# Performance work log

Hardware: AMD Instinct MI355X
Metric: run time of the kernel (lower is better)

Reference implementation:

```python
import jax, jax.numpy as jnp
import numpy as np

B, S, D, H = 4, 2048, 1024, 16
d = D // H
SCALE = d ** -0.5


def setup_inputs() -> dict:
    key = jax.random.key(0)
    k1, k2, k3 = jax.random.split(key, 3)
    x = jax.random.normal(k1, (B, S, D), dtype=jnp.float32)
    # causal keep-mask (True = keep), shape (B, 1, S, S)
    causal = jnp.tril(jnp.ones((S, S), dtype=bool))
    mask = jnp.broadcast_to(causal[None, None, :, :], (B, 1, S, S))
    # nn.Linear(D, 3D, bias=False): weight (3D, D); out_proj weight (D, D)
    w_qkv = jax.random.normal(k2, (3 * D, D), dtype=jnp.float32) * (D ** -0.5)
    w_out = jax.random.normal(k3, (D, D), dtype=jnp.float32) * (D ** -0.5)
    return {"x": x, "mask": mask, "w_qkv": w_qkv, "w_out": w_out}


def reference(x, mask, w_qkv, w_out):
    # qkv projection: y = x @ W^T, split into q, k, v
    qkv = jnp.einsum('bsd,ed->bse', x, w_qkv)  # (B, S, 3D)
    q, k, v = jnp.split(qkv, 3, axis=-1)
    # (B, S, H, d) -> (B, H, S, d)
    q = q.reshape(B, S, H, d).transpose(0, 2, 1, 3)
    k = k.reshape(B, S, H, d).transpose(0, 2, 1, 3)
    v = v.reshape(B, S, H, d).transpose(0, 2, 1, 3)
    # scores (B, H, S, S)
    attn = jnp.einsum('bhqd,bhkd->bhqk', q, k) * SCALE
    attn = jnp.where(mask, attn, -jnp.inf)
    attn = jax.nn.softmax(attn, axis=-1)
    out = jnp.einsum('bhqk,bhkd->bhqd', attn, v)
    out = out.transpose(0, 2, 1, 3).reshape(B, S, D)
    out = jnp.einsum('bsd,ed->bse', out, w_out)
    return out, (k, v)
```

## Files before the change

kernel.cpp:

```cpp
#include <hip/hip_runtime.h>
#include <hip/hip_bf16.h>

typedef __bf16 bf16_t;
typedef bf16_t bf16x8 __attribute__((ext_vector_type(8)));
typedef bf16_t bf16x4 __attribute__((ext_vector_type(4)));
typedef float  f32x4  __attribute__((ext_vector_type(4)));
typedef float  f32x8  __attribute__((ext_vector_type(8)));
typedef float  f32x16 __attribute__((ext_vector_type(16)));

#define B_  4
#define S_  2048
#define D_  1024
#define H_  16
#define HD  64

#define QSCALE 0.1803368801111204f

#define KV_TILE_ELEMS 4096
#define KV_BH_ELEMS   262144

__device__ __forceinline__ void async_copy16(const void* g, void* l) {
    __builtin_amdgcn_global_load_lds((const __attribute__((address_space(1))) void*)g,
                                     (__attribute__((address_space(3))) void*)l,
                                     16, 0, 0);
}

__device__ __forceinline__ float fast_exp2(float x) {
    float r;
    asm("v_exp_f32 %0, %1" : "=v"(r) : "v"(x));
    return r;
}

__global__ __launch_bounds__(256) void cvt_kernel(const float* __restrict__ in,
                                                  bf16_t* __restrict__ out, int n4) {
    int i = blockIdx.x * 256 + threadIdx.x;
    if (i >= n4) return;
    float4 f = ((const float4*)in)[i];
    bf16x4 o = { (bf16_t)f.x, (bf16_t)f.y, (bf16_t)f.z, (bf16_t)f.w };
    ((bf16x4*)out)[i] = o;
}

__device__ __forceinline__ void gemm_tile(const bf16_t* __restrict__ A,
                                          const bf16_t* __restrict__ Bt,
                                          int lda, int ldb, int m0, int n0, int K,
                                          bf16_t* As, bf16_t* Bs, f32x4 acc[4][4]) {
    const int lane = threadIdx.x & 63;
    const int wv   = threadIdx.x >> 6;
    const int wm   = wv >> 1, wn = wv & 1;
    const int r8   = lane >> 3, c8 = lane & 7;
    const int lo   = lane & 15, hi = lane >> 4;
    const int swz  = (lo & 7) * 8;
    const int csw  = (c8 ^ (r8 & 7)) * 8;

    for (int k0 = 0; k0 < K; k0 += 64) {
        #pragma unroll
        for (int i = 0; i < 4; ++i) {
            const int c   = wv * 4 + i;
            const int row = c * 8 + r8;
            async_copy16(A  + (size_t)(m0 + row) * lda + k0 + csw, As + c * 512);
            async_copy16(Bt + (size_t)(n0 + row) * ldb + k0 + csw, Bs + c * 512);
        }
        __syncthreads();
        #pragma unroll
        for (int kk = 0; kk < 2; ++kk) {
            const int kos = (kk * 32 + hi * 8) ^ swz;
            bf16x8 aF[4], bF[4];
            #pragma unroll
            for (int m = 0; m < 4; ++m)
                aF[m] = *(const bf16x8*)(As + (wm * 64 + m * 16 + lo) * 64 + kos);
            #pragma unroll
            for (int n = 0; n < 4; ++n)
                bF[n] = *(const bf16x8*)(Bs + (wn * 64 + n * 16 + lo) * 64 + kos);
            #pragma unroll
            for (int m = 0; m < 4; ++m)
                #pragma unroll
                for (int n = 0; n < 4; ++n)
                    acc[m][n] = __builtin_amdgcn_mfma_f32_16x16x32_bf16(aF[m], bF[n], acc[m][n], 0, 0, 0);
        }
        __syncthreads();
    }
}

__global__ __launch_bounds__(256) void gemm_qkv_kernel(const bf16_t* __restrict__ A,
                                                       const bf16_t* __restrict__ Bt,
                                                       float* __restrict__ out,
                                                       bf16_t* __restrict__ q_ws,
                                                       bf16_t* __restrict__ kv_frag) {
    __shared__ __align__(16) bf16_t As[128 * 64];
    __shared__ __align__(16) bf16_t Bs[128 * 64];
    const int m0 = blockIdx.y * 128, n0 = blockIdx.x * 128;
    const f32x4 zero = {0.f, 0.f, 0.f, 0.f};
    f32x4 acc[4][4];
    #pragma unroll
    for (int m = 0; m < 4; ++m)
        #pragma unroll
        for (int n = 0; n < 4; ++n) acc[m][n] = zero;

    gemm_tile(A, Bt, D_, D_, m0, n0, D_, As, Bs, acc);

    const int lane = threadIdx.x & 63, wv = threadIdx.x >> 6;
    const int wm = wv >> 1, wn = wv & 1;
    const int lo = lane & 15, hi = lane >> 4;
    #pragma unroll
    for (int m = 0; m < 4; ++m) {
        #pragma unroll
        for (int n = 0; n < 4; ++n) {
            const int gcol = n0 + wn * 64 + n * 16 + lo;
            const int sec  = gcol >> 10;
            const int e    = gcol & 1023;
            const int h    = e >> 6, dv = e & 63;
            #pragma unroll
            for (int j4 = 0; j4 < 4; ++j4) {
                const int grow = m0 + wm * 64 + m * 16 + hi * 4 + j4;
                const float v  = acc[m][n][j4];
                const int b = grow >> 11, s = grow & 2047;
                const size_t idx2 = ((((size_t)b * H_ + h) * S_ + s) << 6) + dv;
                if (sec == 0) {
                    q_ws[idx2] = (bf16_t)(v * QSCALE);
                } else if (sec == 1) {
                    out[8388608u + idx2] = v;
                    const int bh   = b * H_ + h;
                    const int tile = s >> 5, ql = s & 31;
                    const int c    = dv >> 4, hb = (dv >> 3) & 1, jj = dv & 7;
                    kv_frag[(((size_t)bh * 64 + tile) * 8 + c) * 512 + hb * 256 + ql * 8 + jj] = (bf16_t)v;
                } else {
                    out[16777216u + idx2] = v;
                }
            }
        }
    }
}

__global__ __launch_bounds__(256) void build_vfrag_kernel(const float* __restrict__ v_f32,
                                                          bf16_t* __restrict__ kv_frag) {
    __shared__ __align__(16) bf16_t T[64][72];
    const int bh = blockIdx.x;
    const int s0 = blockIdx.y * 64;
    const int t  = threadIdx.x;
    {
        const int sl  = t >> 2;
        const int dv0 = (t & 3) * 16;
        const float* src = v_f32 + ((size_t)bh * S_ + s0 + sl) * HD + dv0;
        float tmp[16];
        #pragma unroll
        for (int i = 0; i < 4; ++i) *(float4*)(tmp + i * 4) = ((const float4*)src)[i];
        #pragma unroll
        for (int i = 0; i < 16; ++i) T[dv0 + i][sl] = (bf16_t)tmp[i];
    }
    __syncthreads();
    {
        const int st = t >> 7;
        const int r  = t & 127;
        const int cc = r >> 5;
        const int l  = r & 31;
        const int khi = cc >> 1, hd = cc & 1;
        const int d   = hd * 32 + l;
        const int tile = (s0 >> 5) + st;
        bf16_t* dst = kv_frag + (((size_t)bh * 64 + tile) * 8 + 4 + cc) * 512 + l * 8;
        const int slb = st * 32 + khi * 16;
        *(bf16x8*)(dst)       = *(const bf16x8*)&T[d][slb];
        *(bf16x8*)(dst + 256) = *(const bf16x8*)&T[d][slb + 8];
    }
}

__global__ __launch_bounds__(256) void attn_kernel(const bf16_t* __restrict__ q_ws,
                                                   const bf16_t* __restrict__ kv_frag,
                                                   bf16_t* __restrict__ attn_ws) {
    __shared__ __align__(16) float MRG[2][2][64][20];
    __shared__ float LSUM[2][64];
    __shared__ __align__(16) bf16_t T[2][32][72];
    const int lane = threadIdx.x & 63;
    const int wv   = threadIdx.x >> 6;
    const int blk   = blockIdx.x;
    const int x     = blk & 7;
    const int r     = blk >> 3;
    const int bh    = x + 8 * (r & 7);
    const int pr    = wv >> 1;
    const int khalf = wv & 1;
    const int p     = (r >> 3) * 2 + pr;

    const int ql = lane & 31;
    const int hb = lane >> 5;
    const size_t kv_base = (size_t)bh * (S_ * HD);
    const int b = bh >> 4, h = bh & 15;

    const bf16_t* kvb = kv_frag + (size_t)bh * KV_BH_ELEMS + (size_t)lane * 8;

    auto load_k = [&](int tile, bf16x8 kf[4]) {
        const bf16_t* tp = kvb + (size_t)tile * KV_TILE_ELEMS;
        #pragma unroll
        for (int c = 0; c < 4; ++c) kf[c] = *(const bf16x8*)(tp + c * 512);
    };
    auto load_v = [&](int tile, bf16x8 vf[4]) {
        const bf16_t* tp = kvb + (size_t)tile * KV_TILE_ELEMS + 2048;
        #pragma unroll
        for (int i = 0; i < 4; ++i) vf[i] = *(const bf16x8*)(tp + i * 512);
    };

    #pragma unroll 1
    for (int pass = 0; pass < 2; ++pass) {
        const int qblock = pass ? (63 - p) : p;
        const int q0 = qblock * 32;
        const int nt  = qblock + 1;
        const int mid = nt >> 1;
        const int tstart = khalf ? mid : 0;
        const int tend   = khalf ? nt  : mid;

        bf16x8 qF[4];
        const bf16_t* qrow = q_ws + kv_base + (size_t)(q0 + ql) * HD + hb * 8;
        #pragma unroll
        for (int c = 0; c < 4; ++c) qF[c] = *(const bf16x8*)(qrow + 16 * c);

        f32x16 accT0 = {}, accT1 = {};
        float lsum = 0.f;

        auto compute_tile = [&](const bf16x8 kf[4], const bf16x8 vf[4], bool diag) {
            f32x16 s = {};
            #pragma unroll
            for (int c = 0; c < 4; ++c)
                s = __builtin_amdgcn_mfma_f32_32x32x16_bf16(kf[c], qF[c], s, 0, 0, 0);
            if (diag) {
                #pragma unroll
                for (int rr = 0; rr < 16; ++rr) {
                    const int kloc = (rr & 3) + 8 * (rr >> 2) + 4 * hb;
                    if (kloc > ql) s[rr] = -1e30f;
                }
            }
            #pragma unroll
            for (int rr = 0; rr < 16; ++rr) s[rr] = fast_exp2(s[rr]);
            f32x8 t8 = __builtin_shufflevector(s, s, 0, 1, 2, 3, 4, 5, 6, 7) +
                       __builtin_shufflevector(s, s, 8, 9, 10, 11, 12, 13, 14, 15);
            f32x4 t4 = __builtin_shufflevector(t8, t8, 0, 1, 2, 3) +
                       __builtin_shufflevector(t8, t8, 4, 5, 6, 7);
            lsum += (t4[0] + t4[1]) + (t4[2] + t4[3]);

            unsigned w[8];
            #pragma unroll
            for (int i = 0; i < 8; ++i) {
                unsigned d;
                asm("v_cvt_pk_bf16_f32 %0, %1, %2" : "=v"(d) : "v"(s[2 * i]), "v"(s[2 * i + 1]));
                w[i] = d;
            }
            union { unsigned u[4]; bf16x8 v; } pf0, pf1;
            {
                auto r0 = __builtin_amdgcn_permlane32_swap(w[0], w[2], false, false);
                auto r1 = __builtin_amdgcn_permlane32_swap(w[1], w[3], false, false);
                pf0.u[0] = r0[0]; pf0.u[1] = r1[0]; pf0.u[2] = r0[1]; pf0.u[3] = r1[1];
            }
            {
                auto r0 = __builtin_amdgcn_permlane32_swap(w[4], w[6], false, false);
                auto r1 = __builtin_amdgcn_permlane32_swap(w[5], w[7], false, false);
                pf1.u[0] = r0[0]; pf1.u[1] = r1[0]; pf1.u[2] = r0[1]; pf1.u[3] = r1[1];
            }

            accT0 = __builtin_amdgcn_mfma_f32_32x32x16_bf16(vf[0], pf0.v, accT0, 0, 0, 0);
            accT1 = __builtin_amdgcn_mfma_f32_32x32x16_bf16(vf[1], pf0.v, accT1, 0, 0, 0);
            accT0 = __builtin_amdgcn_mfma_f32_32x32x16_bf16(vf[2], pf1.v, accT0, 0, 0, 0);
            accT1 = __builtin_amdgcn_mfma_f32_32x32x16_bf16(vf[3], pf1.v, accT1, 0, 0, 0);
        };

        int t = tstart;
        for (; t + 1 < tend; t += 2) {
            bf16x8 kA[4], vA[4], kB[4], vB[4];
            load_k(t, kA);
            load_v(t, vA);
            load_k(t + 1, kB);
            load_v(t + 1, vB);
            compute_tile(kA, vA, t == qblock);
            compute_tile(kB, vB, (t + 1) == qblock);
        }
        if (t < tend) {
            bf16x8 kA[4], vA[4];
            load_k(t, kA);
            load_v(t, vA);
            compute_tile(kA, vA, t == qblock);
        }

        if (khalf) {
            *(f32x16*)&MRG[pr][0][lane][0] = accT0;
            *(f32x16*)&MRG[pr][1][lane][0] = accT1;
            LSUM[pr][lane] = lsum;
        }
        __syncthreads();
        if (!khalf) {
            accT0 += *(const f32x16*)&MRG[pr][0][lane][0];
            accT1 += *(const f32x16*)&MRG[pr][1][lane][0];
            lsum  += LSUM[pr][lane];
            const float ltot = lsum + __shfl_xor(lsum, 32, 64);
            const float inv  = 1.0f / ltot;
            #pragma unroll
            for (int rr = 0; rr < 16; ++rr) {
                const int dl = (rr & 3) + 8 * (rr >> 2) + 4 * hb;
                T[pr][ql][dl]      = (bf16_t)(accT0[rr] * inv);
                T[pr][ql][32 + dl] = (bf16_t)(accT1[rr] * inv);
            }
            asm volatile("s_waitcnt lgkmcnt(0)" ::: "memory");
            #pragma unroll
            for (int it = 0; it < 4; ++it) {
                const int ch  = it * 64 + lane;
                const int row = ch >> 3, c8 = ch & 7;
                bf16x8 o = *(const bf16x8*)&T[pr][row][c8 * 8];
                *(bf16x8*)(attn_ws + ((size_t)(b * S_ + q0 + row)) * D_ + h * HD + c8 * 8) = o;
            }
        }
        __syncthreads();
    }
}

__global__ __launch_bounds__(256) void gemm_out_kernel(const bf16_t* __restrict__ A,
                                                       const bf16_t* __restrict__ Bt,
                                                       float* __restrict__ out) {
    __shared__ __align__(16) bf16_t As[128 * 64];
    __shared__ __align__(16) bf16_t Bs[128 * 64];
    const int bid = blockIdx.x;
    const int xcd = bid & 7, idx = bid >> 3;
    const int m0 = idx * 128, n0 = xcd * 128;
    const f32x4 zero = {0.f, 0.f, 0.f, 0.f};
    f32x4 acc[4][4];
    #pragma unroll
    for (int m = 0; m < 4; ++m)
        #pragma unroll
        for (int n = 0; n < 4; ++n) acc[m][n] = zero;

    gemm_tile(A, Bt, D_, D_, m0, n0, D_, As, Bs, acc);

    const int lane = threadIdx.x & 63, wv = threadIdx.x >> 6;
    const int wm = wv >> 1, wn = wv & 1;
    const int lo = lane & 15, hi = lane >> 4;
    #pragma unroll
    for (int m = 0; m < 4; ++m) {
        #pragma unroll
        for (int n = 0; n < 4; ++n) {
            const int gcol = n0 + wn * 64 + n * 16 + lo;
            #pragma unroll
            for (int j = 0; j < 4; ++j) {
                const int grow = m0 + wm * 64 + m * 16 + hi * 4 + j;
                out[(size_t)grow * D_ + gcol] = acc[m][n][j];
            }
        }
    }
}

extern "C" void kernel_launch(void* const* d_in, const int* in_sizes, int n_in,
                              void* d_out, int out_size, void* d_ws, size_t ws_size,
                              hipStream_t stream) {
    (void)in_sizes; (void)n_in; (void)out_size; (void)ws_size;
    const float* x     = (const float*)d_in[0];
    const float* w_qkv = (const float*)d_in[2];
    const float* w_out = (const float*)d_in[3];
    float* out = (float*)d_out;
    char* ws = (char*)d_ws;

    bf16_t* x_bf    = (bf16_t*)(ws);
    bf16_t* wqkv_bf = (bf16_t*)(ws + 16777216);
    bf16_t* wout_bf = (bf16_t*)(ws + 23068672);
    bf16_t* q_ws    = (bf16_t*)(ws + 25165824);
    bf16_t* kv_frag = (bf16_t*)(ws + 41943040);
    bf16_t* attn_ws = (bf16_t*)(ws + 75497472);

    cvt_kernel<<<8192, 256, 0, stream>>>(x, x_bf, 2097152);
    cvt_kernel<<<3072, 256, 0, stream>>>(w_qkv, wqkv_bf, 786432);
    cvt_kernel<<<1024, 256, 0, stream>>>(w_out, wout_bf, 262144);

    gemm_qkv_kernel<<<dim3(24, 64), 256, 0, stream>>>(x_bf, wqkv_bf, out, q_ws, kv_frag);
    build_vfrag_kernel<<<dim3(64, 32), 256, 0, stream>>>(out + 16777216, kv_frag);
    attn_kernel<<<1024, 256, 0, stream>>>(q_ws, kv_frag, attn_ws);
    gemm_out_kernel<<<512, 256, 0, stream>>>(attn_ws, wout_bf, out);
}
```

Before: 183.8 us.

## Triple-buffer GEMM k-loop with async LDS loads and enlarge tiles to 256x128

Restructures the shared GEMM core into a three-stage software pipeline: async global-to-LDS copies for tiles t+1..t+3 are issued while tile t is computed, with explicit vmcnt waits and raw barriers in place of a load-then-sync loop. Block tile grows to 256x128 with 512 threads (8 waves), which halves the grid for both projection GEMMs and drops the XCD-aware block mapping in the output GEMM. This aims to hide global load latency, but uses 144 KB of LDS per block, which limits occupancy to one block per CU, and the hand-written vmcnt counts must exactly match the number of copies issued.

```diff
diff --git a/kernel.cpp b/kernel.cpp
--- a/kernel.cpp
+++ b/kernel.cpp
@@ -18,6 +18,10 @@
 
 #define KV_TILE_ELEMS 4096
 #define KV_BH_ELEMS   262144
+
+#define BM 256
+#define BN 128
+#define BK 64
 
 __device__ __forceinline__ void async_copy16(const void* g, void* l) {
     __builtin_amdgcn_global_load_lds((const __attribute__((address_space(1))) void*)g,
@@ -40,7 +44,7 @@
     ((bf16x4*)out)[i] = o;
 }
 
-__device__ __forceinline__ void gemm_tile(const bf16_t* __restrict__ A,
+__device__ __forceinline__ void gemm_core(const bf16_t* __restrict__ A,
                                           const bf16_t* __restrict__ Bt,
                                           int lda, int ldb, int m0, int n0, int K,
                                           bf16_t* As, bf16_t* Bs, f32x4 acc[4][4]) {
@@ -50,53 +54,78 @@
     const int r8   = lane >> 3, c8 = lane & 7;
     const int lo   = lane & 15, hi = lane >> 4;
     const int swz  = (lo & 7) * 8;
-    const int csw  = (c8 ^ (r8 & 7)) * 8;
-
-    for (int k0 = 0; k0 < K; k0 += 64) {
+    const int csw  = (c8 ^ r8) * 8;
+
+    auto stage = [&](int t, int db) {
+        const int k0 = t * BK;
+        bf16_t* as = As + db * (BM * BK);
+        bf16_t* bs = Bs + db * (BN * BK);
         #pragma unroll
         for (int i = 0; i < 4; ++i) {
-            const int c   = wv * 4 + i;
-            const int row = c * 8 + r8;
-            async_copy16(A  + (size_t)(m0 + row) * lda + k0 + csw, As + c * 512);
-            async_copy16(Bt + (size_t)(n0 + row) * ldb + k0 + csw, Bs + c * 512);
-        }
-        __syncthreads();
+            const int row = i * 64 + wv * 8 + r8;
+            async_copy16(A + (size_t)(m0 + row) * lda + k0 + csw, as + (i * 64 + wv * 8) * BK);
+        }
+        #pragma unroll
+        for (int i = 0; i < 2; ++i) {
+            const int row = i * 64 + wv * 8 + r8;
+            async_copy16(Bt + (size_t)(n0 + row) * ldb + k0 + csw, bs + (i * 64 + wv * 8) * BK);
+        }
+    };
+
+    auto compute = [&](int db) {
+        const bf16_t* as = As + db * (BM * BK);
+        const bf16_t* bs = Bs + db * (BN * BK);
         #pragma unroll
         for (int kk = 0; kk < 2; ++kk) {
             const int kos = (kk * 32 + hi * 8) ^ swz;
             bf16x8 aF[4], bF[4];
             #pragma unroll
             for (int m = 0; m < 4; ++m)
-                aF[m] = *(const bf16x8*)(As + (wm * 64 + m * 16 + lo) * 64 + kos);
+                aF[m] = *(const bf16x8*)(as + (wm * 64 + m * 16 + lo) * BK + kos);
             #pragma unroll
             for (int n = 0; n < 4; ++n)
-                bF[n] = *(const bf16x8*)(Bs + (wn * 64 + n * 16 + lo) * 64 + kos);
+                bF[n] = *(const bf16x8*)(bs + (wn * 64 + n * 16 + lo) * BK + kos);
             #pragma unroll
             for (int m = 0; m < 4; ++m)
                 #pragma unroll
                 for (int n = 0; n < 4; ++n)
                     acc[m][n] = __builtin_amdgcn_mfma_f32_16x16x32_bf16(aF[m], bF[n], acc[m][n], 0, 0, 0);
         }
-        __syncthreads();
-    }
-}
-
-__global__ __launch_bounds__(256) void gemm_qkv_kernel(const bf16_t* __restrict__ A,
+    };
+
+    const int nt = K / BK;
+    stage(0, 0); stage(1, 1); stage(2, 2);
+
+    for (int t = 0; t < nt; ++t) {
+        const int db = t % 3;
+        if (t + 2 < nt)      asm volatile("s_waitcnt vmcnt(12)" ::: "memory");
+        else if (t + 1 < nt) asm volatile("s_waitcnt vmcnt(6)"  ::: "memory");
+        else                 asm volatile("s_waitcnt vmcnt(0)"  ::: "memory");
+        __builtin_amdgcn_s_barrier();
+        __builtin_amdgcn_sched_barrier(0);
+        compute(db);
+        __builtin_amdgcn_sched_barrier(0);
+        __builtin_amdgcn_s_barrier();
+        __builtin_amdgcn_sched_barrier(0);
+        if (t + 3 < nt) stage(t + 3, db);
+    }
+}
+
+__global__ __launch_bounds__(512) void gemm_qkv_kernel(const bf16_t* __restrict__ A,
                                                        const bf16_t* __restrict__ Bt,
                                                        float* __restrict__ out,
                                                        bf16_t* __restrict__ q_ws,
                                                        bf16_t* __restrict__ kv_frag) {
-    __shared__ __align__(16) bf16_t As[128 * 64];
-    __shared__ __align__(16) bf16_t Bs[128 * 64];
-    const int m0 = blockIdx.y * 128, n0 = blockIdx.x * 128;
-    const f32x4 zero = {0.f, 0.f, 0.f, 0.f};
+    __shared__ __align__(16) bf16_t As[3 * BM * BK];
+    __shared__ __align__(16) bf16_t Bs[3 * BN * BK];
+    const int m0 = blockIdx.y * BM, n0 = blockIdx.x * BN;
     f32x4 acc[4][4];
     #pragma unroll
     for (int m = 0; m < 4; ++m)
         #pragma unroll
-        for (int n = 0; n < 4; ++n) acc[m][n] = zero;
-
-    gemm_tile(A, Bt, D_, D_, m0, n0, D_, As, Bs, acc);
+        for (int n = 0; n < 4; ++n) acc[m][n] = f32x4{0.f, 0.f, 0.f, 0.f};
+
+    gemm_core(A, Bt, D_, D_, m0, n0, D_, As, Bs, acc);
 
     const int lane = threadIdx.x & 63, wv = threadIdx.x >> 6;
     const int wm = wv >> 1, wn = wv & 1;
@@ -307,22 +336,19 @@
     }
 }
 
-__global__ __launch_bounds__(256) void gemm_out_kernel(const bf16_t* __restrict__ A,
+__global__ __launch_bounds__(512) void gemm_out_kernel(const bf16_t* __restrict__ A,
                                                        const bf16_t* __restrict__ Bt,
                                                        float* __restrict__ out) {
-    __shared__ __align__(16) bf16_t As[128 * 64];
-    __shared__ __align__(16) bf16_t Bs[128 * 64];
-    const int bid = blockIdx.x;
-    const int xcd = bid & 7, idx = bid >> 3;
-    const int m0 = idx * 128, n0 = xcd * 128;
-    const f32x4 zero = {0.f, 0.f, 0.f, 0.f};
+    __shared__ __align__(16) bf16_t As[3 * BM * BK];
+    __shared__ __align__(16) bf16_t Bs[3 * BN * BK];
+    const int m0 = blockIdx.y * BM, n0 = blockIdx.x * BN;
     f32x4 acc[4][4];
     #pragma unroll
     for (int m = 0; m < 4; ++m)
         #pragma unroll
-        for (int n = 0; n < 4; ++n) acc[m][n] = zero;
-
-    gemm_tile(A, Bt, D_, D_, m0, n0, D_, As, Bs, acc);
+        for (int n = 0; n < 4; ++n) acc[m][n] = f32x4{0.f, 0.f, 0.f, 0.f};
+
+    gemm_core(A, Bt, D_, D_, m0, n0, D_, As, Bs, acc);
 
     const int lane = threadIdx.x & 63, wv = threadIdx.x >> 6;
     const int wm = wv >> 1, wn = wv & 1;
@@ -362,8 +388,8 @@
     cvt_kernel<<<3072, 256, 0, stream>>>(w_qkv, wqkv_bf, 786432);
     cvt_kernel<<<1024, 256, 0, stream>>>(w_out, wout_bf, 262144);
 
-    gemm_qkv_kernel<<<dim3(24, 64), 256, 0, stream>>>(x_bf, wqkv_bf, out, q_ws, kv_frag);
+    gemm_qkv_kernel<<<dim3(24, 32), 512, 0, stream>>>(x_bf, wqkv_bf, out, q_ws, kv_frag);
     build_vfrag_kernel<<<dim3(64, 32), 256, 0, stream>>>(out + 16777216, kv_frag);
     attn_kernel<<<1024, 256, 0, stream>>>(q_ws, kv_frag, attn_ws);
-    gemm_out_kernel<<<512, 256, 0, stream>>>(attn_ws, wout_bf, out);
-}
+    gemm_out_kernel<<<dim3(8, 32), 512, 0, stream>>>(attn_ws, wout_bf, out);
+}
```

After: 184.8 us. Within noise of the previous version (+0.6%).

## Pre-swizzle GEMM operands into MFMA fragment layout and drop LDS staging

Applied to the files above, without the earlier changes.

Conversion kernels now write bf16 operands directly in per-lane MFMA fragment order, and the attention kernel writes its output in the same fragment layout. Both GEMMs then load fragments straight from global memory into registers with no LDS tiles or barriers, and use an XCD-aware block mapping. This removes shared-memory staging and synchronisation, but every wave reloads its fragments from global/L2 with no reuse across waves in a block, so more cache traffic and exposed load latency are likely.

```diff
diff --git a/kernel.cpp b/kernel.cpp
--- a/kernel.cpp
+++ b/kernel.cpp
@@ -19,87 +19,83 @@
 #define KV_TILE_ELEMS 4096
 #define KV_BH_ELEMS   262144
 
-__device__ __forceinline__ void async_copy16(const void* g, void* l) {
-    __builtin_amdgcn_global_load_lds((const __attribute__((address_space(1))) void*)g,
-                                     (__attribute__((address_space(3))) void*)l,
-                                     16, 0, 0);
-}
-
 __device__ __forceinline__ float fast_exp2(float x) {
     float r;
     asm("v_exp_f32 %0, %1" : "=v"(r) : "v"(x));
     return r;
 }
 
-__global__ __launch_bounds__(256) void cvt_kernel(const float* __restrict__ in,
-                                                  bf16_t* __restrict__ out, int n4) {
-    int i = blockIdx.x * 256 + threadIdx.x;
-    if (i >= n4) return;
-    float4 f = ((const float4*)in)[i];
-    bf16x4 o = { (bf16_t)f.x, (bf16_t)f.y, (bf16_t)f.z, (bf16_t)f.w };
-    ((bf16x4*)out)[i] = o;
-}
-
-__device__ __forceinline__ void gemm_tile(const bf16_t* __restrict__ A,
-                                          const bf16_t* __restrict__ Bt,
-                                          int lda, int ldb, int m0, int n0, int K,
-                                          bf16_t* As, bf16_t* Bs, f32x4 acc[4][4]) {
-    const int lane = threadIdx.x & 63;
-    const int wv   = threadIdx.x >> 6;
-    const int wm   = wv >> 1, wn = wv & 1;
-    const int r8   = lane >> 3, c8 = lane & 7;
-    const int lo   = lane & 15, hi = lane >> 4;
-    const int swz  = (lo & 7) * 8;
-    const int csw  = (c8 ^ (r8 & 7)) * 8;
-
-    for (int k0 = 0; k0 < K; k0 += 64) {
-        #pragma unroll
-        for (int i = 0; i < 4; ++i) {
-            const int c   = wv * 4 + i;
-            const int row = c * 8 + r8;
-            async_copy16(A  + (size_t)(m0 + row) * lda + k0 + csw, As + c * 512);
-            async_copy16(Bt + (size_t)(n0 + row) * ldb + k0 + csw, Bs + c * 512);
-        }
-        __syncthreads();
-        #pragma unroll
-        for (int kk = 0; kk < 2; ++kk) {
-            const int kos = (kk * 32 + hi * 8) ^ swz;
-            bf16x8 aF[4], bF[4];
-            #pragma unroll
-            for (int m = 0; m < 4; ++m)
-                aF[m] = *(const bf16x8*)(As + (wm * 64 + m * 16 + lo) * 64 + kos);
+__global__ __launch_bounds__(256) void cvt_frag_kernel(const float* __restrict__ src,
+                                                       bf16_t* __restrict__ dst) {
+    __shared__ __align__(16) bf16_t T[16][1032];
+    const int mt = blockIdx.x;
+    const int t  = threadIdx.x;
+    {
+        const int r  = t >> 4;
+        const int c0 = (t & 15) * 64;
+        const float* s = src + ((size_t)mt * 16 + r) * 1024 + c0;
+        #pragma unroll
+        for (int i = 0; i < 16; ++i) {
+            float4 f = ((const float4*)s)[i];
+            bf16x4 o = { (bf16_t)f.x, (bf16_t)f.y, (bf16_t)f.z, (bf16_t)f.w };
+            *(bf16x4*)&T[r][c0 + i * 4] = o;
+        }
+    }
+    __syncthreads();
+    {
+        bf16_t* base = dst + (size_t)mt * 32 * 512;
+        #pragma unroll
+        for (int i = 0; i < 8; ++i) {
+            const int idx = i * 256 + t;
+            const int ks = idx >> 6, l = idx & 63;
+            bf16x8 o = *(const bf16x8*)&T[l & 15][ks * 32 + ((l >> 4) & 3) * 8];
+            *(bf16x8*)(base + (size_t)ks * 512 + l * 8) = o;
+        }
+    }
+}
+
+__device__ __forceinline__ void frag_gemm_core(const bf16_t* __restrict__ afrag,
+                                               const bf16_t* __restrict__ bfrag,
+                                               int mtBase, int ntBase, int lane,
+                                               f32x4 acc[4][4]) {
+    const bf16_t* ap = afrag + (size_t)mtBase * 32 * 512 + lane * 8;
+    const bf16_t* bp = bfrag + (size_t)ntBase * 32 * 512 + lane * 8;
+    #pragma unroll 1
+    for (int ks = 0; ks < 32; ++ks) {
+        bf16x8 aF[4], bF[4];
+        #pragma unroll
+        for (int i = 0; i < 4; ++i) aF[i] = *(const bf16x8*)(ap + (size_t)(i * 32 + ks) * 512);
+        #pragma unroll
+        for (int i = 0; i < 4; ++i) bF[i] = *(const bf16x8*)(bp + (size_t)(i * 32 + ks) * 512);
+        #pragma unroll
+        for (int m = 0; m < 4; ++m)
             #pragma unroll
             for (int n = 0; n < 4; ++n)
-                bF[n] = *(const bf16x8*)(Bs + (wn * 64 + n * 16 + lo) * 64 + kos);
-            #pragma unroll
-            for (int m = 0; m < 4; ++m)
-                #pragma unroll
-                for (int n = 0; n < 4; ++n)
-                    acc[m][n] = __builtin_amdgcn_mfma_f32_16x16x32_bf16(aF[m], bF[n], acc[m][n], 0, 0, 0);
-        }
-        __syncthreads();
-    }
-}
-
-__global__ __launch_bounds__(256) void gemm_qkv_kernel(const bf16_t* __restrict__ A,
-                                                       const bf16_t* __restrict__ Bt,
+                acc[m][n] = __builtin_amdgcn_mfma_f32_16x16x32_bf16(aF[m], bF[n], acc[m][n], 0, 0, 0);
+    }
+}
+
+__global__ __launch_bounds__(256) void gemm_qkv_kernel(const bf16_t* __restrict__ afrag,
+                                                       const bf16_t* __restrict__ wfrag,
                                                        float* __restrict__ out,
                                                        bf16_t* __restrict__ q_ws,
                                                        bf16_t* __restrict__ kv_frag) {
-    __shared__ __align__(16) bf16_t As[128 * 64];
-    __shared__ __align__(16) bf16_t Bs[128 * 64];
-    const int m0 = blockIdx.y * 128, n0 = blockIdx.x * 128;
-    const f32x4 zero = {0.f, 0.f, 0.f, 0.f};
+    const int bid = blockIdx.x;
+    const int xcd = bid & 7, idx = bid >> 3;
+    const int m_blk = xcd * 8 + (idx & 7);
+    const int n_blk = idx >> 3;
+    const int lane = threadIdx.x & 63, wv = threadIdx.x >> 6;
+    const int wm = wv >> 1, wn = wv & 1;
+
     f32x4 acc[4][4];
     #pragma unroll
     for (int m = 0; m < 4; ++m)
         #pragma unroll
-        for (int n = 0; n < 4; ++n) acc[m][n] = zero;
-
-    gemm_tile(A, Bt, D_, D_, m0, n0, D_, As, Bs, acc);
-
-    const int lane = threadIdx.x & 63, wv = threadIdx.x >> 6;
-    const int wm = wv >> 1, wn = wv & 1;
+        for (int n = 0; n < 4; ++n) acc[m][n] = f32x4{0.f, 0.f, 0.f, 0.f};
+
+    frag_gemm_core(afrag, wfrag, m_blk * 8 + wm * 4, n_blk * 8 + wn * 4, lane, acc);
+
+    const int m0 = m_blk * 128, n0 = n_blk * 128;
     const int lo = lane & 15, hi = lane >> 4;
     #pragma unroll
     for (int m = 0; m < 4; ++m) {
@@ -165,7 +161,7 @@
 
 __global__ __launch_bounds__(256) void attn_kernel(const bf16_t* __restrict__ q_ws,
                                                    const bf16_t* __restrict__ kv_frag,
-                                                   bf16_t* __restrict__ attn_ws) {
+                                                   bf16_t* __restrict__ ofrag) {
     __shared__ __align__(16) float MRG[2][2][64][20];
     __shared__ float LSUM[2][64];
     __shared__ __align__(16) bf16_t T[2][32][72];
@@ -295,37 +291,38 @@
                 T[pr][ql][32 + dl] = (bf16_t)(accT1[rr] * inv);
             }
             asm volatile("s_waitcnt lgkmcnt(0)" ::: "memory");
-            #pragma unroll
-            for (int it = 0; it < 4; ++it) {
-                const int ch  = it * 64 + lane;
-                const int row = ch >> 3, c8 = ch & 7;
-                bf16x8 o = *(const bf16x8*)&T[pr][row][c8 * 8];
-                *(bf16x8*)(attn_ws + ((size_t)(b * S_ + q0 + row)) * D_ + h * HD + c8 * 8) = o;
+            const int mtb = (b * S_ + q0) >> 4;
+            #pragma unroll
+            for (int c = 0; c < 4; ++c) {
+                const int mt_l = c >> 1, ks_l = c & 1;
+                bf16x8 o = *(const bf16x8*)&T[pr][mt_l * 16 + (lane & 15)]
+                                             [ks_l * 32 + ((lane >> 4) & 3) * 8];
+                *(bf16x8*)(ofrag + ((size_t)(mtb + mt_l) * 32 + h * 2 + ks_l) * 512 + lane * 8) = o;
             }
         }
         __syncthreads();
     }
 }
 
-__global__ __launch_bounds__(256) void gemm_out_kernel(const bf16_t* __restrict__ A,
-                                                       const bf16_t* __restrict__ Bt,
+__global__ __launch_bounds__(256) void gemm_out_kernel(const bf16_t* __restrict__ ofrag,
+                                                       const bf16_t* __restrict__ wofrag,
                                                        float* __restrict__ out) {
-    __shared__ __align__(16) bf16_t As[128 * 64];
-    __shared__ __align__(16) bf16_t Bs[128 * 64];
     const int bid = blockIdx.x;
     const int xcd = bid & 7, idx = bid >> 3;
-    const int m0 = idx * 128, n0 = xcd * 128;
-    const f32x4 zero = {0.f, 0.f, 0.f, 0.f};
+    const int m_blk = xcd * 8 + (idx & 7);
+    const int n_blk = idx >> 3;
+    const int lane = threadIdx.x & 63, wv = threadIdx.x >> 6;
+    const int wm = wv >> 1, wn = wv & 1;
+
     f32x4 acc[4][4];
     #pragma unroll
     for (int m = 0; m < 4; ++m)
         #pragma unroll
-        for (int n = 0; n < 4; ++n) acc[m][n] = zero;
-
-    gemm_tile(A, Bt, D_, D_, m0, n0, D_, As, Bs, acc);
-
-    const int lane = threadIdx.x & 63, wv = threadIdx.x >> 6;
-    const int wm = wv >> 1, wn = wv & 1;
+        for (int n = 0; n < 4; ++n) acc[m][n] = f32x4{0.f, 0.f, 0.f, 0.f};
+
+    frag_gemm_core(ofrag, wofrag, m_blk * 8 + wm * 4, n_blk * 8 + wn * 4, lane, acc);
+
+    const int m0 = m_blk * 128, n0 = n_blk * 128;
     const int lo = lane & 15, hi = lane >> 4;
     #pragma unroll
     for (int m = 0; m < 4; ++m) {
@@ -351,19 +348,19 @@
     float* out = (float*)d_out;
     char* ws = (char*)d_ws;
 
-    bf16_t* x_bf    = (bf16_t*)(ws);
-    bf16_t* wqkv_bf = (bf16_t*)(ws + 16777216);
-    bf16_t* wout_bf = (bf16_t*)(ws + 23068672);
+    bf16_t* afrag   = (bf16_t*)(ws);
+    bf16_t* wfrag   = (bf16_t*)(ws + 16777216);
+    bf16_t* wofrag  = (bf16_t*)(ws + 23068672);
     bf16_t* q_ws    = (bf16_t*)(ws + 25165824);
     bf16_t* kv_frag = (bf16_t*)(ws + 41943040);
-    bf16_t* attn_ws = (bf16_t*)(ws + 75497472);
-
-    cvt_kernel<<<8192, 256, 0, stream>>>(x, x_bf, 2097152);
-    cvt_kernel<<<3072, 256, 0, stream>>>(w_qkv, wqkv_bf, 786432);
-    cvt_kernel<<<1024, 256, 0, stream>>>(w_out, wout_bf, 262144);
-
-    gemm_qkv_kernel<<<dim3(24, 64), 256, 0, stream>>>(x_bf, wqkv_bf, out, q_ws, kv_frag);
+    bf16_t* ofrag   = (bf16_t*)(ws + 75497472);
+
+    cvt_frag_kernel<<<512, 256, 0, stream>>>(x, afrag);
+    cvt_frag_kernel<<<192, 256, 0, stream>>>(w_qkv, wfrag);
+    cvt_frag_kernel<<<64, 256, 0, stream>>>(w_out, wofrag);
+
+    gemm_qkv_kernel<<<1536, 256, 0, stream>>>(afrag, wfrag, out, q_ws, kv_frag);
     build_vfrag_kernel<<<dim3(64, 32), 256, 0, stream>>>(out + 16777216, kv_frag);
-    attn_kernel<<<1024, 256, 0, stream>>>(q_ws, kv_frag, attn_ws);
-    gemm_out_kernel<<<512, 256, 0, stream>>>(attn_ws, wout_bf, out);
-}
+    attn_kernel<<<1024, 256, 0, stream>>>(q_ws, kv_frag, ofrag);
+    gemm_out_kernel<<<512, 256, 0, stream>>>(ofrag, wofrag, out);
+}
```

Result: no change. 187.2 us (+1.9%).
